# Performance work log

Hardware: AMD Instinct MI355X
Metric: run time of the kernel (lower is better)

Reference implementation:

```python
import jax, jax.numpy as jnp
import numpy as np

N_PER_G = 18
GRAPHS = 4096
N = GRAPHS * N_PER_G            # 73728 nodes
E = GRAPHS * N_PER_G * (N_PER_G - 1)  # 1253376 edges (fully connected per graph)
F_IN = 1536                     # sfreq * timestep
EPS = 1e-5
SLOPE = 0.01


def _lrelu(v):
    return jnp.where(v >= 0, v, SLOPE * v)


def setup_inputs() -> dict:
    key = jax.random.key(0)
    ks = jax.random.split(key, 32)
    # node features
    x = jax.random.normal(ks[0], (N, F_IN), dtype=jnp.float32)
    # fully-connected edges within each 18-node graph
    src, dst = np.meshgrid(np.arange(N_PER_G), np.arange(N_PER_G), indexing='ij')
    m = src != dst
    src, dst = src[m], dst[m]                      # [306]
    offs = (np.arange(GRAPHS) * N_PER_G)[:, None]
    row = (offs + src[None, :]).reshape(-1)
    col = (offs + dst[None, :]).reshape(-1)
    edge_index = jnp.asarray(np.stack([row, col]), dtype=jnp.int32)  # [2,E]
    edge_weight = jax.random.uniform(ks[1], (E,), dtype=jnp.float32)
    batch = jnp.asarray(np.arange(N) // N_PER_G, dtype=jnp.int32)

    def lin(k, fi, fo):
        kw, kb = jax.random.split(k)
        s = 1.0 / np.sqrt(fi)
        W = jax.random.uniform(kw, (fi, fo), jnp.float32, -s, s)
        b = jax.random.uniform(kb, (fo,), jnp.float32, -s, s)
        return W, b

    def bn(k, f):
        k1, k2 = jax.random.split(k)
        g = jnp.ones((f,), jnp.float32)
        be = jnp.zeros((f,), jnp.float32)
        rm = jax.random.normal(k1, (f,), jnp.float32) * 0.1
        rv = jax.random.uniform(k2, (f,), jnp.float32) + 0.5
        return g, be, rm, rv

    W1, b1 = lin(ks[2], F_IN, 32)
    W2, b2 = lin(ks[3], 32, 64)
    W3, b3 = lin(ks[4], 64, 128)
    g1, be1, rm1, rv1 = bn(ks[5], 32)
    g2, be2, rm2, rv2 = bn(ks[6], 64)
    g3, be3, rm3, rv3 = bn(ks[7], 128)
    fW1, fb1 = lin(ks[8], 128, 64)
    fW2, fb2 = lin(ks[9], 64, 32)
    fW3, fb3 = lin(ks[10], 32, 16)
    fW4, fb4 = lin(ks[11], 16, 1)

    return dict(x=x, edge_index=edge_index, edge_weight=edge_weight, batch=batch,
                W1=W1, b1=b1, g1=g1, be1=be1, rm1=rm1, rv1=rv1,
                W2=W2, b2=b2, g2=g2, be2=be2, rm2=rm2, rv2=rv2,
                W3=W3, b3=b3, g3=g3, be3=be3, rm3=rm3, rv3=rv3,
                fW1=fW1, fb1=fb1, fW2=fW2, fb2=fb2,
                fW3=fW3, fb3=fb3, fW4=fW4, fb4=fb4)


def _gcn_norm(edge_index, edge_weight):
    # add self loops (weight 1), symmetric normalization (PyG GCNConv, improved=False)
    row = jnp.concatenate([edge_index[0], jnp.arange(N, dtype=edge_index.dtype)])
    col = jnp.concatenate([edge_index[1], jnp.arange(N, dtype=edge_index.dtype)])
    w = jnp.concatenate([edge_weight, jnp.ones((N,), edge_weight.dtype)])
    deg = jax.ops.segment_sum(w, col, num_segments=N)
    dinv = jnp.where(deg > 0, jax.lax.rsqrt(jnp.maximum(deg, 1e-30)), 0.0)
    norm = dinv[row] * w * dinv[col]
    return row, col, norm


def _gcn(x, W, b, row, col, norm):
    h = x @ W                                       # [N, Fout]
    out = jax.ops.segment_sum(norm[:, None] * h[row], col, num_segments=N)
    return out + b


def _bn(h, g, be, rm, rv):
    return (h - rm) * jax.lax.rsqrt(rv + EPS) * g + be


def reference(x, edge_index, edge_weight, batch,
              W1, b1, g1, be1, rm1, rv1,
              W2, b2, g2, be2, rm2, rv2,
              W3, b3, g3, be3, rm3, rv3,
              fW1, fb1, fW2, fb2, fW3, fb3, fW4, fb4):
    row, col, norm = _gcn_norm(edge_index, edge_weight)
    h = _lrelu(_bn(_gcn(x, W1, b1, row, col, norm), g1, be1, rm1, rv1))
    h = _lrelu(_bn(_gcn(h, W2, b2, row, col, norm), g2, be2, rm2, rv2))
    h = _lrelu(_bn(_gcn(h, W3, b3, row, col, norm), g3, be3, rm3, rv3))
    # global mean pool over graphs
    sums = jax.ops.segment_sum(h, batch, num_segments=GRAPHS)
    cnt = jax.ops.segment_sum(jnp.ones((N,), h.dtype), batch, num_segments=GRAPHS)
    h = sums / jnp.maximum(cnt, 1.0)[:, None]       # [G,128]
    # MLP head (dropout = identity in eval)
    h = _lrelu(h @ fW1 + fb1)
    h = _lrelu(h @ fW2 + fb2)
    h = _lrelu(h @ fW3 + fb3)
    h = h @ fW4 + fb4
    return h.squeeze(-1)                            # [G]
```

## Files before the change

### kernel.cpp

```cpp
#include <hip/hip_runtime.h>
#include <stdint.h>

#define GRAPHS 4096
#define NPG 18
#define EPERG 306
#define FIN 1536
#define BN_EPS 1e-5f
#define SLOPE 0.01f

using short8  = __attribute__((ext_vector_type(8))) short;
using ushort8 = __attribute__((ext_vector_type(8))) unsigned short;
using f32x4   = __attribute__((ext_vector_type(4))) float;

__device__ __forceinline__ unsigned short f2bf(float f) {
  unsigned u = __builtin_bit_cast(unsigned, f);
  u += 0x7fffu + ((u >> 16) & 1u);
  return (unsigned short)(u >> 16);
}

__global__ void prep_kernel(const float* __restrict__ W1,
    const float* __restrict__ b1, const float* __restrict__ g1,
    const float* __restrict__ be1, const float* __restrict__ rm1, const float* __restrict__ rv1,
    const float* __restrict__ b2, const float* __restrict__ g2,
    const float* __restrict__ be2, const float* __restrict__ rm2, const float* __restrict__ rv2,
    const float* __restrict__ b3, const float* __restrict__ g3,
    const float* __restrict__ be3, const float* __restrict__ rm3, const float* __restrict__ rv3,
    unsigned short* __restrict__ w1frag, float* __restrict__ ab) {
  const int tid = threadIdx.x;
  if (blockIdx.x < 24) {
    int slot = blockIdx.x * 256 + tid;
    int L  = slot & 63;
    int nt = (slot >> 6) & 1;
    int ks = slot >> 7;
    int n  = nt * 16 + (L & 15);
    int kb = ks * 32 + ((L >> 4) << 3);
    ushort8 v;
#pragma unroll
    for (int j = 0; j < 8; ++j) v[j] = f2bf(W1[(kb + j) * 32 + n]);
    *((ushort8*)w1frag + slot) = v;
  } else {
    if (tid < 32) {
      float a = g1[tid] * rsqrtf(rv1[tid] + BN_EPS);
      ab[tid] = a; ab[32 + tid] = (b1[tid] - rm1[tid]) * a + be1[tid];
    }
    if (tid < 64) {
      float a = g2[tid] * rsqrtf(rv2[tid] + BN_EPS);
      ab[64 + tid] = a; ab[128 + tid] = (b2[tid] - rm2[tid]) * a + be2[tid];
    }
    if (tid < 128) {
      float a = g3[tid] * rsqrtf(rv3[tid] + BN_EPS);
      ab[192 + tid] = a; ab[320 + tid] = (b3[tid] - rm3[tid]) * a + be3[tid];
    }
  }
}

union SmemU {
  short xA[2][32][136];
  float Pb[NPG][132];
};

__global__ __launch_bounds__(256, 4) void gcn_main(
    const float* __restrict__ x, const float* __restrict__ ew,
    const float* __restrict__ W2, const float* __restrict__ W3,
    const float* __restrict__ fW1, const float* __restrict__ fb1,
    const float* __restrict__ fW2, const float* __restrict__ fb2,
    const float* __restrict__ fW3, const float* __restrict__ fb3,
    const float* __restrict__ fW4, const float* __restrict__ fb4,
    const unsigned short* __restrict__ w1frag, const float* __restrict__ ab,
    float* __restrict__ out) {
  const int g    = blockIdx.x;
  const int tid  = threadIdx.x;
  const int lane = tid & 63;
  const int wv   = tid >> 6;

  __shared__ float ew_s[EPERG];
  __shared__ float dinv_s[NPG];
  __shared__ float An[NPG][NPG + 1];
  __shared__ SmemU u;
  __shared__ float Hb[NPG][132];
  __shared__ float pooled[128];
  __shared__ float m1[64];
  __shared__ float m2[32];
  __shared__ float m3[16];

  for (int i = tid; i < EPERG; i += 256) ew_s[i] = ew[g * EPERG + i];
  for (int i = tid; i < 2 * 14 * 68; i += 256) {
    int b = i / 952, rem = i - b * 952;
    int r = 18 + rem / 68, c = rem - (rem / 68) * 68;
    ((int*)&u.xA[b][r][0])[c] = 0;
  }
  __syncthreads();

  if (tid < NPG) {
    float deg = 1.0f;
#pragma unroll
    for (int j = 0; j < 17; ++j) {
      int s = j + (j >= tid);
      deg += ew_s[s * 17 + (tid - (tid > s ? 1 : 0))];
    }
    dinv_s[tid] = rsqrtf(deg);
  }
  __syncthreads();

  for (int o = tid; o < NPG * NPG; o += 256) {
    int d = o / NPG, s = o - d * NPG;
    float v;
    if (d == s) v = dinv_s[d] * dinv_s[d];
    else        v = dinv_s[s] * ew_s[s * 17 + (d - (d > s ? 1 : 0))] * dinv_s[d];
    An[d][s] = v;
  }

  const int Mt = wv & 1, Nt = wv >> 1;
  const int arow  = Mt * 16 + (lane & 15);
  const int akoff = (lane >> 4) << 3;
  f32x4 acc = {0.f, 0.f, 0.f, 0.f};
  const float4* __restrict__ x4 = (const float4*)x + (size_t)g * 18 * 384;

  float4 cur[3], nxt[3];
#pragma unroll
  for (int i = 0; i < 3; ++i) {
    int idx = tid + i * 256;
    if (idx < 576) { int r = idx >> 5, c4 = idx & 31; cur[i] = x4[r * 384 + c4]; }
  }

  for (int c = 0; c < 12; ++c) {
    if (c < 11) {
#pragma unroll
      for (int i = 0; i < 3; ++i) {
        int idx = tid + i * 256;
        if (idx < 576) { int r = idx >> 5, c4 = idx & 31; nxt[i] = x4[r * 384 + (c + 1) * 32 + c4]; }
      }
    }
    short8 bf[4];
#pragma unroll
    for (int kk = 0; kk < 4; ++kk)
      bf[kk] = *(const short8*)(w1frag + (size_t)(((c * 4 + kk) * 2 + Nt) * 64 + lane) * 8);

    short (*xb)[136] = u.xA[c & 1];
#pragma unroll
    for (int i = 0; i < 3; ++i) {
      int idx = tid + i * 256;
      if (idx < 576) {
        int r = idx >> 5, c4 = idx & 31;
        ushort4 b;
        b.x = f2bf(cur[i].x); b.y = f2bf(cur[i].y);
        b.z = f2bf(cur[i].z); b.w = f2bf(cur[i].w);
        *(ushort4*)(&xb[r][c4 * 4]) = b;
      }
    }
    __syncthreads();
#pragma unroll
    for (int kk = 0; kk < 4; ++kk) {
      short8 af = *(const short8*)(&xb[arow][kk * 32 + akoff]);
      acc = __builtin_amdgcn_mfma_f32_16x16x32_bf16(af, bf[kk], acc, 0, 0, 0);
    }
#pragma unroll
    for (int i = 0; i < 3; ++i) cur[i] = nxt[i];
  }
  __syncthreads();

  {
    int ccol  = Nt * 16 + (lane & 15);
    int rbase = Mt * 16 + ((lane >> 4) << 2);
#pragma unroll
    for (int q = 0; q < 4; ++q) {
      int rr = rbase + q;
      if (rr < NPG) u.Pb[rr][ccol] = acc[q];
    }
  }
  __syncthreads();

  if (tid < NPG * 8) {
    int d = tid >> 3, c4 = tid & 7;
    f32x4 s = {0.f, 0.f, 0.f, 0.f};
#pragma unroll
    for (int ss = 0; ss < NPG; ++ss) {
      float a = An[d][ss];
      const f32x4 p = *(const f32x4*)&u.Pb[ss][c4 * 4];
#pragma unroll
      for (int j = 0; j < 4; ++j) s[j] = fmaf(a, p[j], s[j]);
    }
    const f32x4 al = *(const f32x4*)(ab + c4 * 4);
    const f32x4 bt = *(const f32x4*)(ab + 32 + c4 * 4);
#pragma unroll
    for (int j = 0; j < 4; ++j) {
      float v = fmaf(s[j], al[j], bt[j]);
      Hb[d][c4 * 4 + j] = v >= 0.f ? v : SLOPE * v;
    }
  }
  __syncthreads();

  for (int o = tid; o < NPG * 16; o += 256) {
    int r = o >> 4, c4 = o & 15;
    f32x4 s = {0.f, 0.f, 0.f, 0.f};
#pragma unroll 8
    for (int k = 0; k < 32; ++k) {
      float h = Hb[r][k];
      const f32x4 w = *(const f32x4*)&W2[k * 64 + c4 * 4];
#pragma unroll
      for (int j = 0; j < 4; ++j) s[j] = fmaf(h, w[j], s[j]);
    }
    *(f32x4*)&u.Pb[r][c4 * 4] = s;
  }
  __syncthreads();
  for (int o = tid; o < NPG * 16; o += 256) {
    int d = o >> 4, c4 = o & 15;
    f32x4 s = {0.f, 0.f, 0.f, 0.f};
#pragma unroll
    for (int ss = 0; ss < NPG; ++ss) {
      float a = An[d][ss];
      const f32x4 p = *(const f32x4*)&u.Pb[ss][c4 * 4];
#pragma unroll
      for (int j = 0; j < 4; ++j) s[j] = fmaf(a, p[j], s[j]);
    }
    const f32x4 al = *(const f32x4*)(ab + 64 + c4 * 4);
    const f32x4 bt = *(const f32x4*)(ab + 128 + c4 * 4);
#pragma unroll
    for (int j = 0; j < 4; ++j) {
      float v = fmaf(s[j], al[j], bt[j]);
      Hb[d][c4 * 4 + j] = v >= 0.f ? v : SLOPE * v;
    }
  }
  __syncthreads();

  for (int o = tid; o < NPG * 32; o += 256) {
    int r = o >> 5, c4 = o & 31;
    f32x4 s = {0.f, 0.f, 0.f, 0.f};
#pragma unroll 8
    for (int k = 0; k < 64; ++k) {
      float h = Hb[r][k];
      const f32x4 w = *(const f32x4*)&W3[k * 128 + c4 * 4];
#pragma unroll
      for (int j = 0; j < 4; ++j) s[j] = fmaf(h, w[j], s[j]);
    }
    *(f32x4*)&u.Pb[r][c4 * 4] = s;
  }
  __syncthreads();
  for (int o = tid; o < NPG * 32; o += 256) {
    int d = o >> 5, c4 = o & 31;
    f32x4 s = {0.f, 0.f, 0.f, 0.f};
#pragma unroll
    for (int ss = 0; ss < NPG; ++ss) {
      float a = An[d][ss];
      const f32x4 p = *(const f32x4*)&u.Pb[ss][c4 * 4];
#pragma unroll
      for (int j = 0; j < 4; ++j) s[j] = fmaf(a, p[j], s[j]);
    }
    const f32x4 al = *(const f32x4*)(ab + 192 + c4 * 4);
    const f32x4 bt = *(const f32x4*)(ab + 320 + c4 * 4);
#pragma unroll
    for (int j = 0; j < 4; ++j) {
      float v = fmaf(s[j], al[j], bt[j]);
      Hb[d][c4 * 4 + j] = v >= 0.f ? v : SLOPE * v;
    }
  }
  __syncthreads();

  if (tid < 128) {
    float s = 0.f;
#pragma unroll
    for (int d = 0; d < NPG; ++d) s += Hb[d][tid];
    pooled[tid] = s * (1.0f / 18.0f);
  }
  __syncthreads();
  if (tid < 64) {
    float s = fb1[tid];
#pragma unroll 8
    for (int k = 0; k < 128; ++k) s = fmaf(pooled[k], fW1[k * 64 + tid], s);
    m1[tid] = s >= 0.f ? s : SLOPE * s;
  }
  __syncthreads();
  if (tid < 32) {
    float s = fb2[tid];
#pragma unroll
    for (int k = 0; k < 64; ++k) s = fmaf(m1[k], fW2[k * 32 + tid], s);
    m2[tid] = s >= 0.f ? s : SLOPE * s;
  }
  __syncthreads();
  if (tid < 16) {
    float s = fb3[tid];
#pragma unroll
    for (int k = 0; k < 32; ++k) s = fmaf(m2[k], fW3[k * 16 + tid], s);
    m3[tid] = s >= 0.f ? s : SLOPE * s;
  }
  __syncthreads();
  if (tid == 0) {
    float s = fb4[0];
#pragma unroll
    for (int k = 0; k < 16; ++k) s = fmaf(m3[k], fW4[k], s);
    out[g] = s;
  }
}

extern "C" void kernel_launch(void* const* d_in, const int* in_sizes, int n_in,
                              void* d_out, int out_size, void* d_ws, size_t ws_size,
                              hipStream_t stream) {
  (void)in_sizes; (void)n_in; (void)out_size; (void)ws_size;
  const float* x   = (const float*)d_in[0];
  const float* ew  = (const float*)d_in[2];
  const float* W1  = (const float*)d_in[4];
  const float* b1  = (const float*)d_in[5];
  const float* g1  = (const float*)d_in[6];
  const float* be1 = (const float*)d_in[7];
  const float* rm1 = (const float*)d_in[8];
  const float* rv1 = (const float*)d_in[9];
  const float* W2  = (const float*)d_in[10];
  const float* b2  = (const float*)d_in[11];
  const float* g2  = (const float*)d_in[12];
  const float* be2 = (const float*)d_in[13];
  const float* rm2 = (const float*)d_in[14];
  const float* rv2 = (const float*)d_in[15];
  const float* W3  = (const float*)d_in[16];
  const float* b3  = (const float*)d_in[17];
  const float* g3  = (const float*)d_in[18];
  const float* be3 = (const float*)d_in[19];
  const float* rm3 = (const float*)d_in[20];
  const float* rv3 = (const float*)d_in[21];
  const float* fW1 = (const float*)d_in[22];
  const float* fb1 = (const float*)d_in[23];
  const float* fW2 = (const float*)d_in[24];
  const float* fb2 = (const float*)d_in[25];
  const float* fW3 = (const float*)d_in[26];
  const float* fb3 = (const float*)d_in[27];
  const float* fW4 = (const float*)d_in[28];
  const float* fb4 = (const float*)d_in[29];

  unsigned short* w1frag = (unsigned short*)d_ws;
  float* ab = (float*)((char*)d_ws + 98304);

  prep_kernel<<<25, 256, 0, stream>>>(W1, b1, g1, be1, rm1, rv1,
                                      b2, g2, be2, rm2, rv2,
                                      b3, g3, be3, rm3, rv3, w1frag, ab);
  gcn_main<<<GRAPHS, 256, 0, stream>>>(x, ew, W2, W3, fW1, fb1, fW2, fb2,
                                       fW3, fb3, fW4, fb4, w1frag, ab,
                                       (float*)d_out);
}
```

Before: 747.0 us.

## Split X·W1 into a standalone dense MFMA GEMM kernel before the per-graph epilogue

The big X·W1 product moves out of the per-graph fused kernel into its own GEMM kernel. Each wave handles 16 contiguous rows across all 32 output columns and loads fp32 directly from global memory into registers, with no LDS staging, no padded rows and no block barriers. The result P goes to a workspace buffer, which a second kernel reads back per graph for the adjacency, BN and MLP stages. This removes the wasted MFMA work on padding rows (18 rows padded to 32) and the per-chunk syncs, at the cost of an extra kernel launch and a global round trip for P.

```diff
diff --git a/kernel.cpp b/kernel.cpp
--- a/kernel.cpp
+++ b/kernel.cpp
@@ -54,40 +54,73 @@
   }
 }
 
-union SmemU {
-  short xA[2][32][136];
-  float Pb[NPG][132];
-};
-
-__global__ __launch_bounds__(256, 4) void gcn_main(
-    const float* __restrict__ x, const float* __restrict__ ew,
+__global__ __launch_bounds__(256, 4) void gemm_xw1(
+    const float* __restrict__ x, const unsigned short* __restrict__ w1frag,
+    float* __restrict__ P) {
+  const int tid  = threadIdx.x;
+  const int lane = tid & 63;
+  const int wv   = tid >> 6;
+  const int rbase = (blockIdx.x * 4 + wv) * 16;
+  const int r    = lane & 15;
+  const int koff = (lane >> 4) << 3;
+
+  const float* __restrict__ rowp = x + (size_t)(rbase + r) * FIN + koff;
+  const short8* __restrict__ wf  = (const short8*)w1frag;
+
+  f32x4 acc0 = {0.f, 0.f, 0.f, 0.f};
+  f32x4 acc1 = {0.f, 0.f, 0.f, 0.f};
+
+#pragma unroll 2
+  for (int ks = 0; ks < 48; ++ks) {
+    const float4* p = (const float4*)(rowp + ks * 32);
+    float4 a0 = p[0], a1 = p[1];
+    short8 b0 = wf[(ks * 2 + 0) * 64 + lane];
+    short8 b1 = wf[(ks * 2 + 1) * 64 + lane];
+    short8 af;
+    af[0] = (short)f2bf(a0.x); af[1] = (short)f2bf(a0.y);
+    af[2] = (short)f2bf(a0.z); af[3] = (short)f2bf(a0.w);
+    af[4] = (short)f2bf(a1.x); af[5] = (short)f2bf(a1.y);
+    af[6] = (short)f2bf(a1.z); af[7] = (short)f2bf(a1.w);
+    acc0 = __builtin_amdgcn_mfma_f32_16x16x32_bf16(af, b0, acc0, 0, 0, 0);
+    acc1 = __builtin_amdgcn_mfma_f32_16x16x32_bf16(af, b1, acc1, 0, 0, 0);
+  }
+
+  const int col = lane & 15;
+  const int rq  = (lane >> 4) << 2;
+  float* __restrict__ Pw = P + (size_t)(rbase + rq) * 32;
+#pragma unroll
+  for (int q = 0; q < 4; ++q) {
+    Pw[q * 32 + col]      = acc0[q];
+    Pw[q * 32 + 16 + col] = acc1[q];
+  }
+}
+
+__global__ __launch_bounds__(256, 4) void gcn_epilogue(
+    const float* __restrict__ P, const float* __restrict__ ew,
     const float* __restrict__ W2, const float* __restrict__ W3,
     const float* __restrict__ fW1, const float* __restrict__ fb1,
     const float* __restrict__ fW2, const float* __restrict__ fb2,
     const float* __restrict__ fW3, const float* __restrict__ fb3,
     const float* __restrict__ fW4, const float* __restrict__ fb4,
-    const unsigned short* __restrict__ w1frag, const float* __restrict__ ab,
-    float* __restrict__ out) {
-  const int g    = blockIdx.x;
-  const int tid  = threadIdx.x;
-  const int lane = tid & 63;
-  const int wv   = tid >> 6;
+    const float* __restrict__ ab, float* __restrict__ out) {
+  const int g   = blockIdx.x;
+  const int tid = threadIdx.x;
 
   __shared__ float ew_s[EPERG];
   __shared__ float dinv_s[NPG];
   __shared__ float An[NPG][NPG + 1];
-  __shared__ SmemU u;
-  __shared__ float Hb[NPG][132];
+  __shared__ __align__(16) float Pb[NPG][132];
+  __shared__ __align__(16) float Hb[NPG][132];
   __shared__ float pooled[128];
   __shared__ float m1[64];
   __shared__ float m2[32];
   __shared__ float m3[16];
 
   for (int i = tid; i < EPERG; i += 256) ew_s[i] = ew[g * EPERG + i];
-  for (int i = tid; i < 2 * 14 * 68; i += 256) {
-    int b = i / 952, rem = i - b * 952;
-    int r = 18 + rem / 68, c = rem - (rem / 68) * 68;
-    ((int*)&u.xA[b][r][0])[c] = 0;
+  if (tid < 144) {
+    int idx = tid * 4;
+    f32x4 v = *(const f32x4*)(P + (size_t)g * NPG * 32 + idx);
+    *(f32x4*)&Pb[idx >> 5][idx & 31] = v;
   }
   __syncthreads();
 
@@ -109,65 +142,6 @@
     else        v = dinv_s[s] * ew_s[s * 17 + (d - (d > s ? 1 : 0))] * dinv_s[d];
     An[d][s] = v;
   }
-
-  const int Mt = wv & 1, Nt = wv >> 1;
-  const int arow  = Mt * 16 + (lane & 15);
-  const int akoff = (lane >> 4) << 3;
-  f32x4 acc = {0.f, 0.f, 0.f, 0.f};
-  const float4* __restrict__ x4 = (const float4*)x + (size_t)g * 18 * 384;
-
-  float4 cur[3], nxt[3];
-#pragma unroll
-  for (int i = 0; i < 3; ++i) {
-    int idx = tid + i * 256;
-    if (idx < 576) { int r = idx >> 5, c4 = idx & 31; cur[i] = x4[r * 384 + c4]; }
-  }
-
-  for (int c = 0; c < 12; ++c) {
-    if (c < 11) {
-#pragma unroll
-      for (int i = 0; i < 3; ++i) {
-        int idx = tid + i * 256;
-        if (idx < 576) { int r = idx >> 5, c4 = idx & 31; nxt[i] = x4[r * 384 + (c + 1) * 32 + c4]; }
-      }
-    }
-    short8 bf[4];
-#pragma unroll
-    for (int kk = 0; kk < 4; ++kk)
-      bf[kk] = *(const short8*)(w1frag + (size_t)(((c * 4 + kk) * 2 + Nt) * 64 + lane) * 8);
-
-    short (*xb)[136] = u.xA[c & 1];
-#pragma unroll
-    for (int i = 0; i < 3; ++i) {
-      int idx = tid + i * 256;
-      if (idx < 576) {
-        int r = idx >> 5, c4 = idx & 31;
-        ushort4 b;
-        b.x = f2bf(cur[i].x); b.y = f2bf(cur[i].y);
-        b.z = f2bf(cur[i].z); b.w = f2bf(cur[i].w);
-        *(ushort4*)(&xb[r][c4 * 4]) = b;
-      }
-    }
-    __syncthreads();
-#pragma unroll
-    for (int kk = 0; kk < 4; ++kk) {
-      short8 af = *(const short8*)(&xb[arow][kk * 32 + akoff]);
-      acc = __builtin_amdgcn_mfma_f32_16x16x32_bf16(af, bf[kk], acc, 0, 0, 0);
-    }
-#pragma unroll
-    for (int i = 0; i < 3; ++i) cur[i] = nxt[i];
-  }
-  __syncthreads();
-
-  {
-    int ccol  = Nt * 16 + (lane & 15);
-    int rbase = Mt * 16 + ((lane >> 4) << 2);
-#pragma unroll
-    for (int q = 0; q < 4; ++q) {
-      int rr = rbase + q;
-      if (rr < NPG) u.Pb[rr][ccol] = acc[q];
-    }
-  }
   __syncthreads();
 
   if (tid < NPG * 8) {
@@ -176,7 +150,7 @@
 #pragma unroll
     for (int ss = 0; ss < NPG; ++ss) {
       float a = An[d][ss];
-      const f32x4 p = *(const f32x4*)&u.Pb[ss][c4 * 4];
+      const f32x4 p = *(const f32x4*)&Pb[ss][c4 * 4];
 #pragma unroll
       for (int j = 0; j < 4; ++j) s[j] = fmaf(a, p[j], s[j]);
     }
@@ -200,7 +174,7 @@
 #pragma unroll
       for (int j = 0; j < 4; ++j) s[j] = fmaf(h, w[j], s[j]);
     }
-    *(f32x4*)&u.Pb[r][c4 * 4] = s;
+    *(f32x4*)&Pb[r][c4 * 4] = s;
   }
   __syncthreads();
   for (int o = tid; o < NPG * 16; o += 256) {
@@ -209,7 +183,7 @@
 #pragma unroll
     for (int ss = 0; ss < NPG; ++ss) {
       float a = An[d][ss];
-      const f32x4 p = *(const f32x4*)&u.Pb[ss][c4 * 4];
+      const f32x4 p = *(const f32x4*)&Pb[ss][c4 * 4];
 #pragma unroll
       for (int j = 0; j < 4; ++j) s[j] = fmaf(a, p[j], s[j]);
     }
@@ -233,7 +207,7 @@
 #pragma unroll
       for (int j = 0; j < 4; ++j) s[j] = fmaf(h, w[j], s[j]);
     }
-    *(f32x4*)&u.Pb[r][c4 * 4] = s;
+    *(f32x4*)&Pb[r][c4 * 4] = s;
   }
   __syncthreads();
   for (int o = tid; o < NPG * 32; o += 256) {
@@ -242,7 +216,7 @@
 #pragma unroll
     for (int ss = 0; ss < NPG; ++ss) {
       float a = An[d][ss];
-      const f32x4 p = *(const f32x4*)&u.Pb[ss][c4 * 4];
+      const f32x4 p = *(const f32x4*)&Pb[ss][c4 * 4];
 #pragma unroll
       for (int j = 0; j < 4; ++j) s[j] = fmaf(a, p[j], s[j]);
     }
@@ -314,8 +288,8 @@
   const float* b3  = (const float*)d_in[17];
   const float* g3  = (const float*)d_in[18];
   const float* be3 = (const float*)d_in[19];
+  const float* rv3 = (const float*)d_in[21];
   const float* rm3 = (const float*)d_in[20];
-  const float* rv3 = (const float*)d_in[21];
   const float* fW1 = (const float*)d_in[22];
   const float* fb1 = (const float*)d_in[23];
   const float* fW2 = (const float*)d_in[24];
@@ -327,11 +301,13 @@
 
   unsigned short* w1frag = (unsigned short*)d_ws;
   float* ab = (float*)((char*)d_ws + 98304);
+  float* P  = (float*)((char*)d_ws + 98304 + 2048);
 
   prep_kernel<<<25, 256, 0, stream>>>(W1, b1, g1, be1, rm1, rv1,
                                       b2, g2, be2, rm2, rv2,
                                       b3, g3, be3, rm3, rv3, w1frag, ab);
-  gcn_main<<<GRAPHS, 256, 0, stream>>>(x, ew, W2, W3, fW1, fb1, fW2, fb2,
-                                       fW3, fb3, fW4, fb4, w1frag, ab,
-                                       (float*)d_out);
-}
+  gemm_xw1<<<GRAPHS * 18 / 64, 256, 0, stream>>>(x, w1frag, P);
+  gcn_epilogue<<<GRAPHS, 256, 0, stream>>>(P, ew, W2, W3, fW1, fb1, fW2, fb2,
+                                           fW3, fb3, fW4, fb4, ab,
+                                           (float*)d_out);
+}
```

Result: slower. 765.3 us (+2.5%).
